# Kernel tuning notes

Measured on AMD Instinct MI355X. Metric: run time of the kernel, lower is better.

## Reference

```python
import jax, jax.numpy as jnp
import numpy as np

B, T, IN_DIM, OUT_DIM, H = 4096, 256, 64, 32, 128

def _linear_params(key, out_f, in_f):
    k1, k2 = jax.random.split(key)
    bound = 1.0 / np.sqrt(in_f)
    W = jax.random.uniform(k1, (out_f, in_f), jnp.float32, -bound, bound)
    b = jax.random.uniform(k2, (out_f,), jnp.float32, -bound, bound)
    return W, b

def _lstm_params(key, input_sz, hidden_sz):
    ks = jax.random.split(key, 4)
    bound = 1.0 / np.sqrt(hidden_sz)
    Wih = jax.random.uniform(ks[0], (4 * hidden_sz, input_sz), jnp.float32, -bound, bound)
    Whh = jax.random.uniform(ks[1], (4 * hidden_sz, hidden_sz), jnp.float32, -bound, bound)
    bih = jax.random.uniform(ks[2], (4 * hidden_sz,), jnp.float32, -bound, bound)
    bhh = jax.random.uniform(ks[3], (4 * hidden_sz,), jnp.float32, -bound, bound)
    return Wih, Whh, bih, bhh

def setup_inputs() -> dict:
    key = jax.random.key(0)
    ks = jax.random.split(key, 9)
    seq = jax.random.normal(ks[0], (B, T, IN_DIM), jnp.float32)
    h1 = jnp.zeros((B, H), jnp.float32); c1 = jnp.zeros((B, H), jnp.float32)
    h2 = jnp.zeros((B, H), jnp.float32); c2 = jnp.zeros((B, H), jnp.float32)
    W_in1, b_in1 = _linear_params(ks[1], 256, IN_DIM)
    W_in2, b_in2 = _linear_params(ks[2], 128, 256)
    W_in3, b_in3 = _linear_params(ks[3], 128, 128)
    Wih1, Whh1, bih1, bhh1 = _lstm_params(ks[4], 128, H)
    Wih2, Whh2, bih2, bhh2 = _lstm_params(ks[5], 128, H)
    W_out1, b_out1 = _linear_params(ks[6], 128, 128)
    W_out2, b_out2 = _linear_params(ks[7], 256, 128)
    W_out3, b_out3 = _linear_params(ks[8], OUT_DIM, 256)
    return dict(seq=seq, h1=h1, c1=c1, h2=h2, c2=c2,
                W_in1=W_in1, b_in1=b_in1, W_in2=W_in2, b_in2=b_in2, W_in3=W_in3, b_in3=b_in3,
                Wih1=Wih1, Whh1=Whh1, bih1=bih1, bhh1=bhh1,
                Wih2=Wih2, Whh2=Whh2, bih2=bih2, bhh2=bhh2,
                W_out1=W_out1, b_out1=b_out1, W_out2=W_out2, b_out2=b_out2, W_out3=W_out3, b_out3=b_out3)

def _lstm_cell(x, h, c, Wih, Whh, bih, bhh):
    # PyTorch LSTMCell: gates ordered i, f, g, o
    g = x @ Wih.T + bih + h @ Whh.T + bhh
    i, f, gg, o = jnp.split(g, 4, axis=-1)
    c_new = jax.nn.sigmoid(f) * c + jax.nn.sigmoid(i) * jnp.tanh(gg)
    h_new = jax.nn.sigmoid(o) * jnp.tanh(c_new)
    return h_new, c_new

def reference(seq, h1, c1, h2, c2,
              W_in1, b_in1, W_in2, b_in2, W_in3, b_in3,
              Wih1, Whh1, bih1, bhh1, Wih2, Whh2, bih2, bhh2,
              W_out1, b_out1, W_out2, b_out2, W_out3, b_out3):
    # fc_in applied to all timesteps at once (same math as per-step)
    x = jax.nn.relu(seq @ W_in1.T + b_in1)
    x = jax.nn.relu(x @ W_in2.T + b_in2)
    x = jax.nn.relu(x @ W_in3.T + b_in3)  # [B, T, 128]

    def step(carry, xt):
        h1, c1, h2, c2 = carry
        h1, c1 = _lstm_cell(xt, h1, c1, Wih1, Whh1, bih1, bhh1)
        h2, c2 = _lstm_cell(h1, h2, c2, Wih2, Whh2, bih2, bhh2)
        return (h1, c1, h2, c2), None

    (h1, c1, h2, c2), _ = jax.lax.scan(step, (h1, c1, h2, c2), jnp.swapaxes(x, 0, 1))

    y = jax.nn.relu(h2 @ W_out1.T + b_out1)
    y = jax.nn.relu(y @ W_out2.T + b_out2)
    return y @ W_out3.T + b_out3  # [B, out_dim]
```

## Files before the change

### kernel.cpp

```cpp
#include <hip/hip_runtime.h>


typedef unsigned short u16;
typedef short bf16x8 __attribute__((ext_vector_type(8)));
typedef float f32x4 __attribute__((ext_vector_type(4)));
typedef unsigned short u16x4 __attribute__((ext_vector_type(4)));

#define MFMA16(a, b, c) __builtin_amdgcn_mfma_f32_16x16x32_bf16((a), (b), (c), 0, 0, 0)

#define GLOAD_LDS(gp, lp) __builtin_amdgcn_global_load_lds( \
    (const __attribute__((address_space(1))) unsigned int*)(const void*)(gp), \
    (__attribute__((address_space(3))) unsigned int*)(void*)(lp), 16, 0, 0)

#define LGKM_BAR do { \
  asm volatile("s_waitcnt lgkmcnt(0)" ::: "memory"); \
  __builtin_amdgcn_sched_barrier(0); \
  __builtin_amdgcn_s_barrier(); \
  __builtin_amdgcn_sched_barrier(0); \
} while (0)

__device__ __forceinline__ u16 f2bf(float f) {
  union { float f; unsigned u; } v; v.f = f;
  return (u16)((v.u + 0x7FFFu + ((v.u >> 16) & 1u)) >> 16);
}
__device__ __forceinline__ float b2f(u16 v) {
  union { unsigned u; float f; } x; x.u = ((unsigned)v) << 16; return x.f;
}
__device__ __forceinline__ float fsig(float x) {
  return __builtin_amdgcn_rcpf(1.0f + __expf(-x));
}
__device__ __forceinline__ float ftanh(float x) {
  return 2.0f * __builtin_amdgcn_rcpf(1.0f + __expf(-2.0f * x)) - 1.0f;
}

#define WHH1_U  0
#define WIH2_U  65536
#define WHH2_U  131072
#define WIH1_U  196608
#define W1_U    262144
#define W2_U    278528
#define W3_U    311296
#define WO1_U   327680
#define WO2_U   344064
#define WO3_U   376832
#define BS1_F   192512
#define BS2_F   193024
#define STH1_U  393216
#define STH2_U  917504
#define C1_F    720896
#define C2_F    1245184
#define G1X_U   4194304
#define TC      32
#define NCH     8


__global__ void prep_kernel(const float* __restrict__ Wih1, const float* __restrict__ Whh1,
                            const float* __restrict__ bih1, const float* __restrict__ bhh1,
                            const float* __restrict__ Wih2, const float* __restrict__ Whh2,
                            const float* __restrict__ bih2, const float* __restrict__ bhh2,
                            const float* __restrict__ W_in1, const float* __restrict__ W_in2,
                            const float* __restrict__ W_in3,
                            const float* __restrict__ W_out1, const float* __restrict__ W_out2,
                            const float* __restrict__ W_out3,
                            const float* __restrict__ h1_in, const float* __restrict__ h2_in,
                            const float* __restrict__ c1_in, const float* __restrict__ c2_in,
                            u16* __restrict__ wsu) {
  float* wsf = (float*)wsu;
  const int N_total = 2490368;
  int stride = gridDim.x * blockDim.x;
  for (int idx = blockIdx.x * blockDim.x + threadIdx.x; idx < N_total; idx += stride) {
    if (idx < 385024) {
      int within = idx & 511;
      int f = idx >> 9;
      int lane = within >> 3, e = within & 7;
      int lr = lane & 15, lg = lane >> 4;
      int k8 = lg * 8 + e;
      float v;
      if (f < 128) {
        int kf = f & 3, g = (f >> 2) & 3, w = f >> 4;
        v = Whh1[(g * 128 + w * 16 + lr) * 128 + kf * 32 + k8];
      } else if (f < 256) {
        int ff = f - 128; int kf = ff & 3, g = (ff >> 2) & 3, w = ff >> 4;
        v = Wih2[(g * 128 + w * 16 + lr) * 128 + kf * 32 + k8];
      } else if (f < 384) {
        int ff = f - 256; int kf = ff & 3, g = (ff >> 2) & 3, w = ff >> 4;
        v = Whh2[(g * 128 + w * 16 + lr) * 128 + kf * 32 + k8];
      } else if (f < 512) {
        int ff = f - 384; int kf = ff & 3, n = ff >> 2;
        v = Wih1[(n * 16 + lr) * 128 + kf * 32 + k8];
      } else if (f < 544) {
        int ff = f - 512; int kf = ff & 1, n = ff >> 1;
        v = W_in1[(n * 16 + lr) * 64 + kf * 32 + k8];
      } else if (f < 608) {
        int ff = f - 544; int kf = ff & 7, n = ff >> 3;
        v = W_in2[(n * 16 + lr) * 256 + kf * 32 + k8];
      } else if (f < 640) {
        int ff = f - 608; int kf = ff & 3, n = ff >> 2;
        v = W_in3[(n * 16 + lr) * 128 + kf * 32 + k8];
      } else if (f < 672) {
        int ff = f - 640; int kf = ff & 3, n = ff >> 2;
        v = W_out1[(n * 16 + lr) * 128 + kf * 32 + k8];
      } else if (f < 736) {
        int ff = f - 672; int kf = ff & 3, n = ff >> 2;
        v = W_out2[(n * 16 + lr) * 128 + kf * 32 + k8];
      } else {
        int ff = f - 736; int kf = ff & 7, n = ff >> 3;
        v = W_out3[(n * 16 + lr) * 256 + kf * 32 + k8];
      }
      wsu[idx] = f2bf(v);
    } else if (idx < 385536) {
      int i = idx - 385024; wsf[BS1_F + i] = bih1[i] + bhh1[i];
    } else if (idx < 386048) {
      int i = idx - 385536; wsf[BS2_F + i] = bih2[i] + bhh2[i];
    } else if (idx < 393216) {
    } else if (idx < 917504) {
      int i = idx - 393216; wsu[STH1_U + i] = f2bf(h1_in[i]);
    } else if (idx < 1441792) {
      int i = idx - 917504; wsu[STH2_U + i] = f2bf(h2_in[i]);
    } else if (idx < 1966080) {
      int i = idx - 1441792; wsf[C1_F + i] = c1_in[i];
    } else {
      int i = idx - 1966080; wsf[C2_F + i] = c2_in[i];
    }
  }
}

__global__ __launch_bounds__(256, 2)
void fc_chunk(const float* __restrict__ seq,
              const float* __restrict__ b_in1, const float* __restrict__ b_in2,
              const float* __restrict__ b_in3,
              u16* __restrict__ wsu, int t0) {
  __shared__ u16 SEQs[4096];
  __shared__ u16 F1s[16384];
  __shared__ u16 F2s[8192];
  __shared__ u16 XLs[8192];
  const int tid = threadIdx.x;
  const int wid = tid >> 6, lane = tid & 63;
  const int lr = lane & 15, lg = lane >> 4;
  const int bid_t = blockIdx.x & 1, bid_b = blockIdx.x >> 1;
  const int b0c = bid_b * 4, t0c = t0 + bid_t * 16;
  const float* bs1f = (const float*)wsu + BS1_F;

#pragma unroll
  for (int i = 0; i < 4; ++i) {
    int f = i * 1024 + tid * 4;
    int rho = f >> 6, k = f & 63;
    int b = b0c + (rho >> 4), tt = t0c + (rho & 15);
    float4 v = *(const float4*)(seq + ((size_t)b * 256 + tt) * 64 + k);
    u16x4 o = { f2bf(v.x), f2bf(v.y), f2bf(v.z), f2bf(v.w) };
    *(u16x4*)&SEQs[(rho * 64 + k) ^ ((rho & 7) << 3)] = o;
  }
  __syncthreads();

  {
    f32x4 a1[4][4] = {};
#pragma unroll
    for (int kf = 0; kf < 2; ++kf) {
      bf16x8 A[4];
#pragma unroll
      for (int rt = 0; rt < 4; ++rt) {
        int r = 16 * rt + lr;
        A[rt] = *(const bf16x8*)&SEQs[(r * 64 + (kf * 4 + lg) * 8) ^ ((r & 7) << 3)];
      }
#pragma unroll
      for (int n = 0; n < 4; ++n) {
        bf16x8 B = *(const bf16x8*)(wsu + W1_U + (size_t)(((4 * wid + n) * 2 + kf) * 512) + lane * 8);
#pragma unroll
        for (int rt = 0; rt < 4; ++rt) a1[rt][n] = MFMA16(A[rt], B, a1[rt][n]);
      }
    }
#pragma unroll
    for (int n = 0; n < 4; ++n) {
      float bb = b_in1[(4 * wid + n) * 16 + lr];
#pragma unroll
      for (int rt = 0; rt < 4; ++rt)
#pragma unroll
        for (int j = 0; j < 4; ++j) {
          int r = 16 * rt + lg * 4 + j, c = (4 * wid + n) * 16 + lr;
          F1s[(r * 256 + c) ^ ((r & 7) << 3)] = f2bf(fmaxf(a1[rt][n][j] + bb, 0.f));
        }
    }
  }
  __syncthreads();

  {
    f32x4 a2[4][2] = {};
#pragma unroll
    for (int kf = 0; kf < 8; ++kf) {
      bf16x8 A[4];
#pragma unroll
      for (int rt = 0; rt < 4; ++rt) {
        int r = 16 * rt + lr;
        A[rt] = *(const bf16x8*)&F1s[(r * 256 + (kf * 4 + lg) * 8) ^ ((r & 7) << 3)];
      }
#pragma unroll
      for (int n = 0; n < 2; ++n) {
        bf16x8 B = *(const bf16x8*)(wsu + W2_U + (size_t)(((2 * wid + n) * 8 + kf) * 512) + lane * 8);
#pragma unroll
        for (int rt = 0; rt < 4; ++rt) a2[rt][n] = MFMA16(A[rt], B, a2[rt][n]);
      }
    }
#pragma unroll
    for (int n = 0; n < 2; ++n) {
      float bb = b_in2[(2 * wid + n) * 16 + lr];
#pragma unroll
      for (int rt = 0; rt < 4; ++rt)
#pragma unroll
        for (int j = 0; j < 4; ++j) {
          int r = 16 * rt + lg * 4 + j, c = (2 * wid + n) * 16 + lr;
          F2s[(r * 128 + c) ^ ((r & 7) << 3)] = f2bf(fmaxf(a2[rt][n][j] + bb, 0.f));
        }
    }
  }
  __syncthreads();

  {
    f32x4 a3[4][2] = {};
#pragma unroll
    for (int kf = 0; kf < 4; ++kf) {
      bf16x8 A[4];
#pragma unroll
      for (int rt = 0; rt < 4; ++rt) {
        int r = 16 * rt + lr;
        A[rt] = *(const bf16x8*)&F2s[(r * 128 + (kf * 4 + lg) * 8) ^ ((r & 7) << 3)];
      }
#pragma unroll
      for (int n = 0; n < 2; ++n) {
        bf16x8 B = *(const bf16x8*)(wsu + W3_U + (size_t)(((2 * wid + n) * 4 + kf) * 512) + lane * 8);
#pragma unroll
        for (int rt = 0; rt < 4; ++rt) a3[rt][n] = MFMA16(A[rt], B, a3[rt][n]);
      }
    }
#pragma unroll
    for (int n = 0; n < 2; ++n) {
      float bb = b_in3[(2 * wid + n) * 16 + lr];
#pragma unroll
      for (int rt = 0; rt < 4; ++rt)
#pragma unroll
        for (int j = 0; j < 4; ++j) {
          int r = 16 * rt + lg * 4 + j, c = (2 * wid + n) * 16 + lr;
          XLs[(r * 128 + c) ^ ((r & 7) << 3)] = f2bf(fmaxf(a3[rt][n][j] + bb, 0.f));
        }
    }
  }
  __syncthreads();

  {
    f32x4 a4[4][8] = {};
#pragma unroll
    for (int kf = 0; kf < 4; ++kf) {
      bf16x8 A[4];
#pragma unroll
      for (int rt = 0; rt < 4; ++rt) {
        int r = 16 * rt + lr;
        A[rt] = *(const bf16x8*)&XLs[(r * 128 + (kf * 4 + lg) * 8) ^ ((r & 7) << 3)];
      }
#pragma unroll
      for (int n = 0; n < 8; ++n) {
        bf16x8 B = *(const bf16x8*)(wsu + WIH1_U + (size_t)(((wid * 8 + n) * 4 + kf) * 512) + lane * 8);
#pragma unroll
        for (int rt = 0; rt < 4; ++rt) a4[rt][n] = MFMA16(A[rt], B, a4[rt][n]);
      }
    }
    const int blk = bid_b >> 2, slg = bid_b & 3;
#pragma unroll
    for (int n = 0; n < 8; ++n) {
      float bb = bs1f[(wid * 8 + n) * 16 + lr];
#pragma unroll
      for (int j = 0; j < 4; ++j) {
        int tl = bid_t * 16 + lg * 4 + j;
        u16x4 o = { f2bf(a4[0][n][j] + bb), f2bf(a4[1][n][j] + bb),
                    f2bf(a4[2][n][j] + bb), f2bf(a4[3][n][j] + bb) };
        size_t au = (size_t)G1X_U +
            ((((((size_t)tl * 256 + blk) * 4 + slg) * 4 + wid) * 8 + n) * 16 + lr) * 4;
        *(u16x4*)(wsu + au) = o;
      }
    }
  }
}

__global__ __launch_bounds__(512, 1)
void scan_chunk(u16* __restrict__ wsu, float* __restrict__ out,
                const float* __restrict__ b_out1, const float* __restrict__ b_out2,
                const float* __restrict__ b_out3, int last) {
  __shared__ u16 Wl[65536];
  __shared__ u16 H1d[2][2048], H2d[2][2048];

  float* wsf = (float*)wsu;
  const int tid = threadIdx.x;
  const int wid = tid >> 6, lane = tid & 63;
  const int lr = lane & 15, lg = lane >> 4;
  const int b0 = blockIdx.x * 16;
  const int blkid = blockIdx.x;
  const int r5 = tid >> 5, c5 = (tid & 31) * 4;
  const int swl = (r5 * 128 + c5) ^ ((r5 & 7) << 3);

  bf16x8 wA[4][4], wB[4][4];
#pragma unroll
  for (int g = 0; g < 4; ++g)
#pragma unroll
    for (int kf = 0; kf < 4; ++kf) {
      wA[g][kf] = *(const bf16x8*)(wsu + WHH1_U + (size_t)(((wid * 4 + g) * 4 + kf) * 512) + lane * 8);
      wB[g][kf] = *(const bf16x8*)(wsu + WIH2_U + (size_t)(((wid * 4 + g) * 4 + kf) * 512) + lane * 8);
    }
#pragma unroll
  for (int g = 0; g < 4; ++g)
#pragma unroll
    for (int kf = 0; kf < 4; ++kf) {
      asm volatile("" : "+a"(wA[g][kf]));
      asm volatile("" : "+a"(wB[g][kf]));
    }

#pragma unroll
  for (int i = 0; i < 16; ++i)
    GLOAD_LDS(wsu + WHH2_U + (wid * 16 + i) * 512 + lane * 8, &Wl[(wid * 16 + i) * 512]);

  *(u16x4*)&H1d[0][swl] = *(const u16x4*)(wsu + STH1_U + (size_t)(b0 + r5) * 128 + c5);
  *(u16x4*)&H2d[0][swl] = *(const u16x4*)(wsu + STH2_U + (size_t)(b0 + r5) * 128 + c5);
  float cs1[4], cs2[4], bc2[4];
#pragma unroll
  for (int j = 0; j < 4; ++j) {
    cs1[j] = wsf[C1_F + (size_t)(b0 + lg * 4 + j) * 128 + 16 * wid + lr];
    cs2[j] = wsf[C2_F + (size_t)(b0 + lg * 4 + j) * 128 + 16 * wid + lr];
  }
#pragma unroll
  for (int g = 0; g < 4; ++g) bc2[g] = wsf[BS2_F + g * 128 + 16 * wid + lr];

  u16x4 gx[4];
#pragma unroll
  for (int g = 0; g < 4; ++g)
    gx[g] = *(const u16x4*)(wsu + G1X_U +
        ((((((size_t)0 * 256 + blkid) * 4 + lg) * 4 + g) * 8 + wid) * 16 + lr) * 4);

  __syncthreads();

  auto frag = [&](const u16* buf, int kg) -> bf16x8 {
    return *(const bf16x8*)&buf[(lr * 128 + kg * 8) ^ ((lr & 7) << 3)];
  };

#pragma unroll 2
  for (int tl = 0; tl < TC; ++tl) {
    const int p = tl & 1, q = p ^ 1;

    f32x4 acc[4];
#pragma unroll
    for (int g = 0; g < 4; ++g)
      acc[g] = (f32x4){ b2f(gx[g][0]), b2f(gx[g][1]), b2f(gx[g][2]), b2f(gx[g][3]) };
    if (tl < TC - 1) {
#pragma unroll
      for (int g = 0; g < 4; ++g)
        gx[g] = *(const u16x4*)(wsu + G1X_U +
            ((((((size_t)(tl + 1) * 256 + blkid) * 4 + lg) * 4 + g) * 8 + wid) * 16 + lr) * 4);
    }
    bf16x8 h1f[4];
#pragma unroll
    for (int kf = 0; kf < 4; ++kf) h1f[kf] = frag(H1d[p], kf * 4 + lg);
#pragma unroll
    for (int kf = 0; kf < 4; ++kf)
#pragma unroll
      for (int g = 0; g < 4; ++g) acc[g] = MFMA16(h1f[kf], wA[g][kf], acc[g]);
    u16 hv[4];
#pragma unroll
    for (int j = 0; j < 4; ++j) {
      float cn = fsig(acc[1][j]) * cs1[j] + fsig(acc[0][j]) * ftanh(acc[2][j]);
      cs1[j] = cn;
      hv[j] = f2bf(fsig(acc[3][j]) * ftanh(cn));
    }
#pragma unroll
    for (int j = 0; j < 4; ++j) {
      int r = lg * 4 + j;
      H1d[q][(r * 128 + 16 * wid + lr) ^ ((r & 7) << 3)] = hv[j];
    }
    LGKM_BAR;

    f32x4 acd[4];
#pragma unroll
    for (int g = 0; g < 4; ++g) acd[g] = (f32x4){ bc2[g], bc2[g], bc2[g], bc2[g] };
#pragma unroll
    for (int kf = 0; kf < 4; ++kf) {
      bf16x8 h1n = frag(H1d[q], kf * 4 + lg);
#pragma unroll
      for (int g = 0; g < 4; ++g) acd[g] = MFMA16(h1n, wB[g][kf], acd[g]);
    }
#pragma unroll
    for (int kf = 0; kf < 4; ++kf) {
      bf16x8 h2f = frag(H2d[p], kf * 4 + lg);
#pragma unroll
      for (int g = 0; g < 4; ++g) {
        bf16x8 B = *(const bf16x8*)&Wl[(((wid * 4 + g) * 4 + kf) * 512) + lane * 8];
        acd[g] = MFMA16(h2f, B, acd[g]);
      }
    }
#pragma unroll
    for (int j = 0; j < 4; ++j) {
      float cn = fsig(acd[1][j]) * cs2[j] + fsig(acd[0][j]) * ftanh(acd[2][j]);
      cs2[j] = cn;
      hv[j] = f2bf(fsig(acd[3][j]) * ftanh(cn));
    }
#pragma unroll
    for (int j = 0; j < 4; ++j) {
      int r = lg * 4 + j;
      H2d[q][(r * 128 + 16 * wid + lr) ^ ((r & 7) << 3)] = hv[j];
    }
  }
  LGKM_BAR;

  if (!last) {
    *(u16x4*)(wsu + STH1_U + (size_t)(b0 + r5) * 128 + c5) = *(const u16x4*)&H1d[0][swl];
    *(u16x4*)(wsu + STH2_U + (size_t)(b0 + r5) * 128 + c5) = *(const u16x4*)&H2d[0][swl];
#pragma unroll
    for (int j = 0; j < 4; ++j) {
      wsf[C1_F + (size_t)(b0 + lg * 4 + j) * 128 + 16 * wid + lr] = cs1[j];
      wsf[C2_F + (size_t)(b0 + lg * 4 + j) * 128 + 16 * wid + lr] = cs2[j];
    }
  } else {
    {
      f32x4 y1 = {};
#pragma unroll
      for (int kf = 0; kf < 4; ++kf) {
        bf16x8 A = frag(H2d[0], kf * 4 + lg);
        bf16x8 B = *(const bf16x8*)(wsu + WO1_U + (size_t)((wid * 4 + kf) * 512) + lane * 8);
        y1 = MFMA16(A, B, y1);
      }
      float bo1 = b_out1[wid * 16 + lr];
      LGKM_BAR;
#pragma unroll
      for (int j = 0; j < 4; ++j) {
        int r = lg * 4 + j;
        H1d[1][(r * 128 + 16 * wid + lr) ^ ((r & 7) << 3)] = f2bf(fmaxf(y1[j] + bo1, 0.f));
      }
      LGKM_BAR;
    }
    {
      f32x4 y2[2] = {};
#pragma unroll
      for (int kf = 0; kf < 4; ++kf) {
        bf16x8 A = frag(H1d[1], kf * 4 + lg);
#pragma unroll
        for (int n = 0; n < 2; ++n) {
          bf16x8 B = *(const bf16x8*)(wsu + WO2_U + (size_t)(((2 * wid + n) * 4 + kf) * 512) + lane * 8);
          y2[n] = MFMA16(A, B, y2[n]);
        }
      }
      LGKM_BAR;
#pragma unroll
      for (int n = 0; n < 2; ++n)
#pragma unroll
        for (int j = 0; j < 4; ++j) {
          int c = (2 * wid + n) * 16 + lr;
          float v = fmaxf(y2[n][j] + b_out2[c], 0.f);
          u16* buf = (c < 128) ? &H2d[1][0] : &H1d[0][0];
          int cc = c & 127, r = lg * 4 + j;
          buf[(r * 128 + cc) ^ ((r & 7) << 3)] = f2bf(v);
        }
      LGKM_BAR;
    }
    if (wid < 2) {
      f32x4 y3 = {};
#pragma unroll
      for (int kf = 0; kf < 8; ++kf) {
        const u16* ab = (kf < 4) ? &H2d[1][0] : &H1d[0][0];
        bf16x8 A = frag(ab, (kf & 3) * 4 + lg);
        bf16x8 B = *(const bf16x8*)(wsu + WO3_U + (size_t)((wid * 8 + kf) * 512) + lane * 8);
        y3 = MFMA16(A, B, y3);
      }
      float bo3 = b_out3[wid * 16 + lr];
#pragma unroll
      for (int j = 0; j < 4; ++j)
        out[(size_t)(b0 + lg * 4 + j) * 32 + wid * 16 + lr] = y3[j] + bo3;
    }
  }
}

extern "C" void kernel_launch(void* const* d_in, const int* in_sizes, int n_in,
                              void* d_out, int out_size, void* d_ws, size_t ws_size,
                              hipStream_t stream) {
  (void)in_sizes; (void)n_in; (void)out_size; (void)ws_size;
  const float* seq    = (const float*)d_in[0];
  const float* h1     = (const float*)d_in[1];
  const float* c1     = (const float*)d_in[2];
  const float* h2     = (const float*)d_in[3];
  const float* c2     = (const float*)d_in[4];
  const float* W_in1  = (const float*)d_in[5];
  const float* b_in1  = (const float*)d_in[6];
  const float* W_in2  = (const float*)d_in[7];
  const float* b_in2  = (const float*)d_in[8];
  const float* W_in3  = (const float*)d_in[9];
  const float* b_in3  = (const float*)d_in[10];
  const float* Wih1   = (const float*)d_in[11];
  const float* Whh1   = (const float*)d_in[12];
  const float* bih1   = (const float*)d_in[13];
  const float* bhh1   = (const float*)d_in[14];
  const float* Wih2   = (const float*)d_in[15];
  const float* Whh2   = (const float*)d_in[16];
  const float* bih2   = (const float*)d_in[17];
  const float* bhh2   = (const float*)d_in[18];
  const float* W_out1 = (const float*)d_in[19];
  const float* b_out1 = (const float*)d_in[20];
  const float* W_out2 = (const float*)d_in[21];
  const float* b_out2 = (const float*)d_in[22];
  const float* W_out3 = (const float*)d_in[23];
  const float* b_out3 = (const float*)d_in[24];
  u16* wsu = (u16*)d_ws;
  float* out = (float*)d_out;

  hipLaunchKernelGGL(prep_kernel, dim3(512), dim3(256), 0, stream,
                     Wih1, Whh1, bih1, bhh1, Wih2, Whh2, bih2, bhh2,
                     W_in1, W_in2, W_in3, W_out1, W_out2, W_out3,
                     h1, h2, c1, c2, wsu);
  for (int k = 0; k < NCH; ++k) {
    hipLaunchKernelGGL(fc_chunk, dim3(2048), dim3(256), 0, stream,
                       seq, b_in1, b_in2, b_in3, wsu, k * TC);
    hipLaunchKernelGGL(scan_chunk, dim3(256), dim3(512), 0, stream,
                       wsu, out, b_out1, b_out2, b_out3, (k == NCH - 1) ? 1 : 0);
  }
}
```

Measured before the change: 1.669 ms.

## Fuse FC and scan chunks into one kernel overlapping next-chunk FC with scan

```diff
diff --git a/kernel.cpp b/kernel.cpp
--- a/kernel.cpp
+++ b/kernel.cpp
@@ -50,9 +50,8 @@
 #define C1_F    720896
 #define C2_F    1245184
 #define G1X_U   4194304
+#define G1X_SLOT 67108864
 #define TC      32
-#define NCH     8
-
 
 __global__ void prep_kernel(const float* __restrict__ Wih1, const float* __restrict__ Whh1,
                             const float* __restrict__ bih1, const float* __restrict__ bhh1,
@@ -125,349 +124,401 @@
   }
 }
 
-__global__ __launch_bounds__(256, 2)
-void fc_chunk(const float* __restrict__ seq,
-              const float* __restrict__ b_in1, const float* __restrict__ b_in2,
-              const float* __restrict__ b_in3,
-              u16* __restrict__ wsu, int t0) {
-  __shared__ u16 SEQs[4096];
-  __shared__ u16 F1s[16384];
-  __shared__ u16 F2s[8192];
-  __shared__ u16 XLs[8192];
-  const int tid = threadIdx.x;
-  const int wid = tid >> 6, lane = tid & 63;
-  const int lr = lane & 15, lg = lane >> 4;
-  const int bid_t = blockIdx.x & 1, bid_b = blockIdx.x >> 1;
-  const int b0c = bid_b * 4, t0c = t0 + bid_t * 16;
-  const float* bs1f = (const float*)wsu + BS1_F;
-
-#pragma unroll
-  for (int i = 0; i < 4; ++i) {
-    int f = i * 1024 + tid * 4;
-    int rho = f >> 6, k = f & 63;
-    int b = b0c + (rho >> 4), tt = t0c + (rho & 15);
-    float4 v = *(const float4*)(seq + ((size_t)b * 256 + tt) * 64 + k);
-    u16x4 o = { f2bf(v.x), f2bf(v.y), f2bf(v.z), f2bf(v.w) };
-    *(u16x4*)&SEQs[(rho * 64 + k) ^ ((rho & 7) << 3)] = o;
-  }
-  __syncthreads();
-
-  {
-    f32x4 a1[4][4] = {};
-#pragma unroll
-    for (int kf = 0; kf < 2; ++kf) {
-      bf16x8 A[4];
-#pragma unroll
-      for (int rt = 0; rt < 4; ++rt) {
-        int r = 16 * rt + lr;
-        A[rt] = *(const bf16x8*)&SEQs[(r * 64 + (kf * 4 + lg) * 8) ^ ((r & 7) << 3)];
-      }
-#pragma unroll
-      for (int n = 0; n < 4; ++n) {
-        bf16x8 B = *(const bf16x8*)(wsu + W1_U + (size_t)(((4 * wid + n) * 2 + kf) * 512) + lane * 8);
-#pragma unroll
-        for (int rt = 0; rt < 4; ++rt) a1[rt][n] = MFMA16(A[rt], B, a1[rt][n]);
-      }
-    }
-#pragma unroll
-    for (int n = 0; n < 4; ++n) {
-      float bb = b_in1[(4 * wid + n) * 16 + lr];
-#pragma unroll
-      for (int rt = 0; rt < 4; ++rt)
-#pragma unroll
-        for (int j = 0; j < 4; ++j) {
-          int r = 16 * rt + lg * 4 + j, c = (4 * wid + n) * 16 + lr;
-          F1s[(r * 256 + c) ^ ((r & 7) << 3)] = f2bf(fmaxf(a1[rt][n][j] + bb, 0.f));
-        }
-    }
-  }
-  __syncthreads();
-
-  {
-    f32x4 a2[4][2] = {};
-#pragma unroll
-    for (int kf = 0; kf < 8; ++kf) {
-      bf16x8 A[4];
-#pragma unroll
-      for (int rt = 0; rt < 4; ++rt) {
-        int r = 16 * rt + lr;
-        A[rt] = *(const bf16x8*)&F1s[(r * 256 + (kf * 4 + lg) * 8) ^ ((r & 7) << 3)];
-      }
-#pragma unroll
-      for (int n = 0; n < 2; ++n) {
-        bf16x8 B = *(const bf16x8*)(wsu + W2_U + (size_t)(((2 * wid + n) * 8 + kf) * 512) + lane * 8);
-#pragma unroll
-        for (int rt = 0; rt < 4; ++rt) a2[rt][n] = MFMA16(A[rt], B, a2[rt][n]);
-      }
-    }
-#pragma unroll
-    for (int n = 0; n < 2; ++n) {
-      float bb = b_in2[(2 * wid + n) * 16 + lr];
-#pragma unroll
-      for (int rt = 0; rt < 4; ++rt)
-#pragma unroll
-        for (int j = 0; j < 4; ++j) {
-          int r = 16 * rt + lg * 4 + j, c = (2 * wid + n) * 16 + lr;
-          F2s[(r * 128 + c) ^ ((r & 7) << 3)] = f2bf(fmaxf(a2[rt][n][j] + bb, 0.f));
-        }
-    }
-  }
-  __syncthreads();
-
-  {
-    f32x4 a3[4][2] = {};
-#pragma unroll
-    for (int kf = 0; kf < 4; ++kf) {
-      bf16x8 A[4];
-#pragma unroll
-      for (int rt = 0; rt < 4; ++rt) {
-        int r = 16 * rt + lr;
-        A[rt] = *(const bf16x8*)&F2s[(r * 128 + (kf * 4 + lg) * 8) ^ ((r & 7) << 3)];
-      }
-#pragma unroll
-      for (int n = 0; n < 2; ++n) {
-        bf16x8 B = *(const bf16x8*)(wsu + W3_U + (size_t)(((2 * wid + n) * 4 + kf) * 512) + lane * 8);
-#pragma unroll
-        for (int rt = 0; rt < 4; ++rt) a3[rt][n] = MFMA16(A[rt], B, a3[rt][n]);
-      }
-    }
-#pragma unroll
-    for (int n = 0; n < 2; ++n) {
-      float bb = b_in3[(2 * wid + n) * 16 + lr];
-#pragma unroll
-      for (int rt = 0; rt < 4; ++rt)
-#pragma unroll
-        for (int j = 0; j < 4; ++j) {
-          int r = 16 * rt + lg * 4 + j, c = (2 * wid + n) * 16 + lr;
-          XLs[(r * 128 + c) ^ ((r & 7) << 3)] = f2bf(fmaxf(a3[rt][n][j] + bb, 0.f));
-        }
-    }
-  }
-  __syncthreads();
-
-  {
-    f32x4 a4[4][8] = {};
-#pragma unroll
-    for (int kf = 0; kf < 4; ++kf) {
-      bf16x8 A[4];
-#pragma unroll
-      for (int rt = 0; rt < 4; ++rt) {
-        int r = 16 * rt + lr;
-        A[rt] = *(const bf16x8*)&XLs[(r * 128 + (kf * 4 + lg) * 8) ^ ((r & 7) << 3)];
-      }
-#pragma unroll
-      for (int n = 0; n < 8; ++n) {
-        bf16x8 B = *(const bf16x8*)(wsu + WIH1_U + (size_t)(((wid * 8 + n) * 4 + kf) * 512) + lane * 8);
-#pragma unroll
-        for (int rt = 0; rt < 4; ++rt) a4[rt][n] = MFMA16(A[rt], B, a4[rt][n]);
-      }
-    }
-    const int blk = bid_b >> 2, slg = bid_b & 3;
-#pragma unroll
-    for (int n = 0; n < 8; ++n) {
-      float bb = bs1f[(wid * 8 + n) * 16 + lr];
-#pragma unroll
-      for (int j = 0; j < 4; ++j) {
-        int tl = bid_t * 16 + lg * 4 + j;
-        u16x4 o = { f2bf(a4[0][n][j] + bb), f2bf(a4[1][n][j] + bb),
-                    f2bf(a4[2][n][j] + bb), f2bf(a4[3][n][j] + bb) };
-        size_t au = (size_t)G1X_U +
-            ((((((size_t)tl * 256 + blk) * 4 + slg) * 4 + wid) * 8 + n) * 16 + lr) * 4;
-        *(u16x4*)(wsu + au) = o;
-      }
-    }
-  }
-}
-
 __global__ __launch_bounds__(512, 1)
-void scan_chunk(u16* __restrict__ wsu, float* __restrict__ out,
-                const float* __restrict__ b_out1, const float* __restrict__ b_out2,
-                const float* __restrict__ b_out3, int last) {
-  __shared__ u16 Wl[65536];
-  __shared__ u16 H1d[2][2048], H2d[2][2048];
-
+void fused_kernel(const float* __restrict__ seq,
+                  const float* __restrict__ b_in1, const float* __restrict__ b_in2,
+                  const float* __restrict__ b_in3,
+                  const float* __restrict__ b_out1, const float* __restrict__ b_out2,
+                  const float* __restrict__ b_out3,
+                  u16* __restrict__ wsu, float* __restrict__ out,
+                  int nscan, int scan_chunk, int fc_chunk, int last) {
+  __shared__ u16 SH[77824];
   float* wsf = (float*)wsu;
   const int tid = threadIdx.x;
-  const int wid = tid >> 6, lane = tid & 63;
-  const int lr = lane & 15, lg = lane >> 4;
-  const int b0 = blockIdx.x * 16;
-  const int blkid = blockIdx.x;
-  const int r5 = tid >> 5, c5 = (tid & 31) * 4;
-  const int swl = (r5 * 128 + c5) ^ ((r5 & 7) << 3);
-
-  bf16x8 wA[4][4], wB[4][4];
-#pragma unroll
-  for (int g = 0; g < 4; ++g)
-#pragma unroll
-    for (int kf = 0; kf < 4; ++kf) {
-      wA[g][kf] = *(const bf16x8*)(wsu + WHH1_U + (size_t)(((wid * 4 + g) * 4 + kf) * 512) + lane * 8);
-      wB[g][kf] = *(const bf16x8*)(wsu + WIH2_U + (size_t)(((wid * 4 + g) * 4 + kf) * 512) + lane * 8);
-    }
-#pragma unroll
-  for (int g = 0; g < 4; ++g)
-#pragma unroll
-    for (int kf = 0; kf < 4; ++kf) {
-      asm volatile("" : "+a"(wA[g][kf]));
-      asm volatile("" : "+a"(wB[g][kf]));
-    }
-
-#pragma unroll
-  for (int i = 0; i < 16; ++i)
-    GLOAD_LDS(wsu + WHH2_U + (wid * 16 + i) * 512 + lane * 8, &Wl[(wid * 16 + i) * 512]);
-
-  *(u16x4*)&H1d[0][swl] = *(const u16x4*)(wsu + STH1_U + (size_t)(b0 + r5) * 128 + c5);
-  *(u16x4*)&H2d[0][swl] = *(const u16x4*)(wsu + STH2_U + (size_t)(b0 + r5) * 128 + c5);
-  float cs1[4], cs2[4], bc2[4];
-#pragma unroll
-  for (int j = 0; j < 4; ++j) {
-    cs1[j] = wsf[C1_F + (size_t)(b0 + lg * 4 + j) * 128 + 16 * wid + lr];
-    cs2[j] = wsf[C2_F + (size_t)(b0 + lg * 4 + j) * 128 + 16 * wid + lr];
-  }
-#pragma unroll
-  for (int g = 0; g < 4; ++g) bc2[g] = wsf[BS2_F + g * 128 + 16 * wid + lr];
-
-  u16x4 gx[4];
-#pragma unroll
-  for (int g = 0; g < 4; ++g)
-    gx[g] = *(const u16x4*)(wsu + G1X_U +
-        ((((((size_t)0 * 256 + blkid) * 4 + lg) * 4 + g) * 8 + wid) * 16 + lr) * 4);
-
-  __syncthreads();
-
-  auto frag = [&](const u16* buf, int kg) -> bf16x8 {
-    return *(const bf16x8*)&buf[(lr * 128 + kg * 8) ^ ((lr & 7) << 3)];
-  };
+  const int bid = blockIdx.x;
+
+  if (bid < nscan) {
+    u16* WL  = SH;
+    u16* H1D = SH + 65536;
+    u16* H2S = SH + 73728;
+    const int wid = tid >> 6, lane = tid & 63;
+    const int lr = lane & 15, lg = lane >> 4;
+    const int b0 = bid * 32;
+
+    bf16x8 wA[4][4], wB[4][4];
+#pragma unroll
+    for (int g = 0; g < 4; ++g)
+#pragma unroll
+      for (int kf = 0; kf < 4; ++kf) {
+        size_t fo = (size_t)(((wid * 4 + g) * 4 + kf) * 512) + lane * 8;
+        wA[g][kf] = *(const bf16x8*)(wsu + WHH1_U + fo);
+        wB[g][kf] = *(const bf16x8*)(wsu + WIH2_U + fo);
+      }
+#pragma unroll
+    for (int g = 0; g < 4; ++g)
+#pragma unroll
+      for (int kf = 0; kf < 4; ++kf) {
+        asm volatile("" : "+a"(wA[g][kf]));
+        asm volatile("" : "+a"(wB[g][kf]));
+      }
+#pragma unroll
+    for (int i = 0; i < 16; ++i)
+      GLOAD_LDS(wsu + WHH2_U + (wid * 16 + i) * 512 + lane * 8, &WL[(wid * 16 + i) * 512]);
+
+    const int srow = tid >> 4, sg8 = tid & 15;
+    const int sws = (srow * 128 + sg8 * 8) ^ ((srow & 7) << 3);
+    *(bf16x8*)&H1D[sws] = *(const bf16x8*)(wsu + STH1_U + (size_t)(b0 + srow) * 128 + sg8 * 8);
+    *(bf16x8*)&H2S[sws] = *(const bf16x8*)(wsu + STH2_U + (size_t)(b0 + srow) * 128 + sg8 * 8);
+    float cs1[2][4], cs2[2][4], bc2[4];
+#pragma unroll
+    for (int rt = 0; rt < 2; ++rt)
+#pragma unroll
+      for (int j = 0; j < 4; ++j) {
+        size_t off = (size_t)(b0 + 16 * rt + lg * 4 + j) * 128 + 16 * wid + lr;
+        cs1[rt][j] = wsf[C1_F + off];
+        cs2[rt][j] = wsf[C2_F + off];
+      }
+#pragma unroll
+    for (int g = 0; g < 4; ++g) bc2[g] = wsf[BS2_F + g * 128 + 16 * wid + lr];
+
+    const u16* gp = wsu + G1X_U + (size_t)(scan_chunk & 1) * G1X_SLOT +
+                    (size_t)(2 * bid) * 8192 + lg * 2048 + wid * 64 + lr * 4;
+    u16x4 gx[2][4];
+#pragma unroll
+    for (int rt = 0; rt < 2; ++rt)
+#pragma unroll
+      for (int g = 0; g < 4; ++g)
+        gx[rt][g] = *(const u16x4*)(gp + rt * 8192 + g * 512);
+
+    __syncthreads();
+
+    auto frag = [&](const u16* buf, int rt, int kg) -> bf16x8 {
+      return *(const bf16x8*)&buf[((16 * rt + lr) * 128 + kg * 8) ^ ((lr & 7) << 3)];
+    };
 
 #pragma unroll 2
-  for (int tl = 0; tl < TC; ++tl) {
-    const int p = tl & 1, q = p ^ 1;
-
-    f32x4 acc[4];
-#pragma unroll
-    for (int g = 0; g < 4; ++g)
-      acc[g] = (f32x4){ b2f(gx[g][0]), b2f(gx[g][1]), b2f(gx[g][2]), b2f(gx[g][3]) };
-    if (tl < TC - 1) {
-#pragma unroll
-      for (int g = 0; g < 4; ++g)
-        gx[g] = *(const u16x4*)(wsu + G1X_U +
-            ((((((size_t)(tl + 1) * 256 + blkid) * 4 + lg) * 4 + g) * 8 + wid) * 16 + lr) * 4);
-    }
-    bf16x8 h1f[4];
-#pragma unroll
-    for (int kf = 0; kf < 4; ++kf) h1f[kf] = frag(H1d[p], kf * 4 + lg);
-#pragma unroll
-    for (int kf = 0; kf < 4; ++kf)
-#pragma unroll
-      for (int g = 0; g < 4; ++g) acc[g] = MFMA16(h1f[kf], wA[g][kf], acc[g]);
-    u16 hv[4];
-#pragma unroll
-    for (int j = 0; j < 4; ++j) {
-      float cn = fsig(acc[1][j]) * cs1[j] + fsig(acc[0][j]) * ftanh(acc[2][j]);
-      cs1[j] = cn;
-      hv[j] = f2bf(fsig(acc[3][j]) * ftanh(cn));
-    }
-#pragma unroll
-    for (int j = 0; j < 4; ++j) {
-      int r = lg * 4 + j;
-      H1d[q][(r * 128 + 16 * wid + lr) ^ ((r & 7) << 3)] = hv[j];
+    for (int tl = 0; tl < TC; ++tl) {
+      const int p = tl & 1, q = p ^ 1;
+      u16* H1p = H1D + p * 4096;
+      u16* H1q = H1D + q * 4096;
+
+      f32x4 acc[2][4];
+#pragma unroll
+      for (int rt = 0; rt < 2; ++rt)
+#pragma unroll
+        for (int g = 0; g < 4; ++g)
+          acc[rt][g] = (f32x4){ b2f(gx[rt][g][0]), b2f(gx[rt][g][1]),
+                                b2f(gx[rt][g][2]), b2f(gx[rt][g][3]) };
+      if (tl < TC - 1) {
+        const u16* gpt = gp + (size_t)(tl + 1) * 2097152;
+#pragma unroll
+        for (int rt = 0; rt < 2; ++rt)
+#pragma unroll
+          for (int g = 0; g < 4; ++g)
+            gx[rt][g] = *(const u16x4*)(gpt + rt * 8192 + g * 512);
+      }
+#pragma unroll
+      for (int kf = 0; kf < 4; ++kf) {
+        bf16x8 a0 = frag(H1p, 0, kf * 4 + lg);
+        bf16x8 a1 = frag(H1p, 1, kf * 4 + lg);
+#pragma unroll
+        for (int g = 0; g < 4; ++g) {
+          acc[0][g] = MFMA16(a0, wA[g][kf], acc[0][g]);
+          acc[1][g] = MFMA16(a1, wA[g][kf], acc[1][g]);
+        }
+      }
+#pragma unroll
+      for (int rt = 0; rt < 2; ++rt)
+#pragma unroll
+        for (int j = 0; j < 4; ++j) {
+          float cn = fsig(acc[rt][1][j]) * cs1[rt][j] + fsig(acc[rt][0][j]) * ftanh(acc[rt][2][j]);
+          cs1[rt][j] = cn;
+          int r = 16 * rt + lg * 4 + j;
+          H1q[(r * 128 + 16 * wid + lr) ^ ((r & 7) << 3)] = f2bf(fsig(acc[rt][3][j]) * ftanh(cn));
+        }
+      LGKM_BAR;
+
+      f32x4 acd[2][4];
+#pragma unroll
+      for (int rt = 0; rt < 2; ++rt)
+#pragma unroll
+        for (int g = 0; g < 4; ++g)
+          acd[rt][g] = (f32x4){ bc2[g], bc2[g], bc2[g], bc2[g] };
+#pragma unroll
+      for (int kf = 0; kf < 4; ++kf) {
+        bf16x8 a0 = frag(H1q, 0, kf * 4 + lg);
+        bf16x8 a1 = frag(H1q, 1, kf * 4 + lg);
+#pragma unroll
+        for (int g = 0; g < 4; ++g) {
+          acd[0][g] = MFMA16(a0, wB[g][kf], acd[0][g]);
+          acd[1][g] = MFMA16(a1, wB[g][kf], acd[1][g]);
+        }
+      }
+#pragma unroll
+      for (int kf = 0; kf < 4; ++kf) {
+        bf16x8 h0 = frag(H2S, 0, kf * 4 + lg);
+        bf16x8 h1 = frag(H2S, 1, kf * 4 + lg);
+#pragma unroll
+        for (int g = 0; g < 4; ++g) {
+          bf16x8 B = *(const bf16x8*)&WL[(((wid * 4 + g) * 4 + kf) * 512) + lane * 8];
+          acd[0][g] = MFMA16(h0, B, acd[0][g]);
+          acd[1][g] = MFMA16(h1, B, acd[1][g]);
+        }
+      }
+      u16 hv[2][4];
+#pragma unroll
+      for (int rt = 0; rt < 2; ++rt)
+#pragma unroll
+        for (int j = 0; j < 4; ++j) {
+          float cn = fsig(acd[rt][1][j]) * cs2[rt][j] + fsig(acd[rt][0][j]) * ftanh(acd[rt][2][j]);
+          cs2[rt][j] = cn;
+          hv[rt][j] = f2bf(fsig(acd[rt][3][j]) * ftanh(cn));
+        }
+      LGKM_BAR;
+#pragma unroll
+      for (int rt = 0; rt < 2; ++rt)
+#pragma unroll
+        for (int j = 0; j < 4; ++j) {
+          int r = 16 * rt + lg * 4 + j;
+          H2S[(r * 128 + 16 * wid + lr) ^ ((r & 7) << 3)] = hv[rt][j];
+        }
     }
     LGKM_BAR;
 
-    f32x4 acd[4];
-#pragma unroll
-    for (int g = 0; g < 4; ++g) acd[g] = (f32x4){ bc2[g], bc2[g], bc2[g], bc2[g] };
-#pragma unroll
-    for (int kf = 0; kf < 4; ++kf) {
-      bf16x8 h1n = frag(H1d[q], kf * 4 + lg);
-#pragma unroll
-      for (int g = 0; g < 4; ++g) acd[g] = MFMA16(h1n, wB[g][kf], acd[g]);
-    }
-#pragma unroll
-    for (int kf = 0; kf < 4; ++kf) {
-      bf16x8 h2f = frag(H2d[p], kf * 4 + lg);
-#pragma unroll
-      for (int g = 0; g < 4; ++g) {
-        bf16x8 B = *(const bf16x8*)&Wl[(((wid * 4 + g) * 4 + kf) * 512) + lane * 8];
-        acd[g] = MFMA16(h2f, B, acd[g]);
-      }
-    }
-#pragma unroll
-    for (int j = 0; j < 4; ++j) {
-      float cn = fsig(acd[1][j]) * cs2[j] + fsig(acd[0][j]) * ftanh(acd[2][j]);
-      cs2[j] = cn;
-      hv[j] = f2bf(fsig(acd[3][j]) * ftanh(cn));
-    }
-#pragma unroll
-    for (int j = 0; j < 4; ++j) {
-      int r = lg * 4 + j;
-      H2d[q][(r * 128 + 16 * wid + lr) ^ ((r & 7) << 3)] = hv[j];
-    }
-  }
-  LGKM_BAR;
-
-  if (!last) {
-    *(u16x4*)(wsu + STH1_U + (size_t)(b0 + r5) * 128 + c5) = *(const u16x4*)&H1d[0][swl];
-    *(u16x4*)(wsu + STH2_U + (size_t)(b0 + r5) * 128 + c5) = *(const u16x4*)&H2d[0][swl];
-#pragma unroll
-    for (int j = 0; j < 4; ++j) {
-      wsf[C1_F + (size_t)(b0 + lg * 4 + j) * 128 + 16 * wid + lr] = cs1[j];
-      wsf[C2_F + (size_t)(b0 + lg * 4 + j) * 128 + 16 * wid + lr] = cs2[j];
+    if (!last) {
+      *(bf16x8*)(wsu + STH1_U + (size_t)(b0 + srow) * 128 + sg8 * 8) = *(const bf16x8*)&H1D[sws];
+      *(bf16x8*)(wsu + STH2_U + (size_t)(b0 + srow) * 128 + sg8 * 8) = *(const bf16x8*)&H2S[sws];
+#pragma unroll
+      for (int rt = 0; rt < 2; ++rt)
+#pragma unroll
+        for (int j = 0; j < 4; ++j) {
+          size_t off = (size_t)(b0 + 16 * rt + lg * 4 + j) * 128 + 16 * wid + lr;
+          wsf[C1_F + off] = cs1[rt][j];
+          wsf[C2_F + off] = cs2[rt][j];
+        }
+    } else {
+      u16* Y1b  = H1D + 4096;
+      u16* Y2lo = H2S;
+      u16* Y2hi = H1D;
+      {
+        f32x4 y1[2] = {};
+#pragma unroll
+        for (int kf = 0; kf < 4; ++kf) {
+          bf16x8 B = *(const bf16x8*)(wsu + WO1_U + (size_t)((wid * 4 + kf) * 512) + lane * 8);
+          y1[0] = MFMA16(frag(H2S, 0, kf * 4 + lg), B, y1[0]);
+          y1[1] = MFMA16(frag(H2S, 1, kf * 4 + lg), B, y1[1]);
+        }
+        float bo1 = b_out1[wid * 16 + lr];
+        LGKM_BAR;
+#pragma unroll
+        for (int rt = 0; rt < 2; ++rt)
+#pragma unroll
+          for (int j = 0; j < 4; ++j) {
+            int r = 16 * rt + lg * 4 + j;
+            Y1b[(r * 128 + 16 * wid + lr) ^ ((r & 7) << 3)] = f2bf(fmaxf(y1[rt][j] + bo1, 0.f));
+          }
+        LGKM_BAR;
+      }
+      {
+        f32x4 y2[2][2] = {};
+#pragma unroll
+        for (int kf = 0; kf < 4; ++kf) {
+          bf16x8 a0 = frag(Y1b, 0, kf * 4 + lg);
+          bf16x8 a1 = frag(Y1b, 1, kf * 4 + lg);
+#pragma unroll
+          for (int n = 0; n < 2; ++n) {
+            bf16x8 B = *(const bf16x8*)(wsu + WO2_U + (size_t)(((2 * wid + n) * 4 + kf) * 512) + lane * 8);
+            y2[0][n] = MFMA16(a0, B, y2[0][n]);
+            y2[1][n] = MFMA16(a1, B, y2[1][n]);
+          }
+        }
+        LGKM_BAR;
+#pragma unroll
+        for (int rt = 0; rt < 2; ++rt)
+#pragma unroll
+          for (int n = 0; n < 2; ++n)
+#pragma unroll
+            for (int j = 0; j < 4; ++j) {
+              int c = (2 * wid + n) * 16 + lr;
+              float v = fmaxf(y2[rt][n][j] + b_out2[c], 0.f);
+              u16* buf = (c < 128) ? Y2lo : Y2hi;
+              int cc = c & 127, r = 16 * rt + lg * 4 + j;
+              buf[(r * 128 + cc) ^ ((r & 7) << 3)] = f2bf(v);
+            }
+        LGKM_BAR;
+      }
+      if (wid < 4) {
+        int rt = wid >> 1, ci = wid & 1;
+        f32x4 y3 = {};
+#pragma unroll
+        for (int kf = 0; kf < 8; ++kf) {
+          const u16* ab = (kf < 4) ? Y2lo : Y2hi;
+          bf16x8 A = frag(ab, rt, (kf & 3) * 4 + lg);
+          bf16x8 B = *(const bf16x8*)(wsu + WO3_U + (size_t)((ci * 8 + kf) * 512) + lane * 8);
+          y3 = MFMA16(A, B, y3);
+        }
+        float bo3 = b_out3[ci * 16 + lr];
+#pragma unroll
+        for (int j = 0; j < 4; ++j)
+          out[(size_t)(b0 + 16 * rt + lg * 4 + j) * 32 + ci * 16 + lr] = y3[j] + bo3;
+      }
     }
   } else {
-    {
-      f32x4 y1 = {};
-#pragma unroll
-      for (int kf = 0; kf < 4; ++kf) {
-        bf16x8 A = frag(H2d[0], kf * 4 + lg);
-        bf16x8 B = *(const bf16x8*)(wsu + WO1_U + (size_t)((wid * 4 + kf) * 512) + lane * 8);
-        y1 = MFMA16(A, B, y1);
-      }
-      float bo1 = b_out1[wid * 16 + lr];
-      LGKM_BAR;
-#pragma unroll
-      for (int j = 0; j < 4; ++j) {
-        int r = lg * 4 + j;
-        H1d[1][(r * 128 + 16 * wid + lr) ^ ((r & 7) << 3)] = f2bf(fmaxf(y1[j] + bo1, 0.f));
-      }
-      LGKM_BAR;
-    }
-    {
-      f32x4 y2[2] = {};
-#pragma unroll
-      for (int kf = 0; kf < 4; ++kf) {
-        bf16x8 A = frag(H1d[1], kf * 4 + lg);
+    const int sub = tid >> 8, stid = tid & 255;
+    u16* S = SH + sub * 36864;
+    u16* SEQs = S;
+    u16* F1s  = S + 4096;
+    u16* F2s  = S + 20480;
+    u16* XLs  = S + 28672;
+    const int wid = stid >> 6, lane = stid & 63;
+    const int lr = lane & 15, lg = lane >> 4;
+    const int t0 = fc_chunk * TC;
+    const size_t g1b = (size_t)G1X_U + (size_t)(fc_chunk & 1) * G1X_SLOT;
+    const float* bs1f = (const float*)wsu + BS1_F;
+    const int nunits = 2 * (gridDim.x - nscan);
+    const int unit = (bid - nscan) * 2 + sub;
+
+    for (int tile = unit; tile < 2048; tile += nunits) {
+      const int bid_t = tile & 1, bid_b = tile >> 1;
+      const int b0c = bid_b * 4, t0c = t0 + bid_t * 16;
+
+#pragma unroll
+      for (int i = 0; i < 4; ++i) {
+        int f = i * 1024 + stid * 4;
+        int rho = f >> 6, k = f & 63;
+        int b = b0c + (rho >> 4), tt = t0c + (rho & 15);
+        float4 v = *(const float4*)(seq + ((size_t)b * 256 + tt) * 64 + k);
+        u16x4 o = { f2bf(v.x), f2bf(v.y), f2bf(v.z), f2bf(v.w) };
+        *(u16x4*)&SEQs[(rho * 64 + k) ^ ((rho & 7) << 3)] = o;
+      }
+      __syncthreads();
+
+      {
+        f32x4 a1[4][4] = {};
+#pragma unroll
+        for (int kf = 0; kf < 2; ++kf) {
+          bf16x8 A[4];
+#pragma unroll
+          for (int rt = 0; rt < 4; ++rt) {
+            int r = 16 * rt + lr;
+            A[rt] = *(const bf16x8*)&SEQs[(r * 64 + (kf * 4 + lg) * 8) ^ ((r & 7) << 3)];
+          }
+#pragma unroll
+          for (int n = 0; n < 4; ++n) {
+            bf16x8 B = *(const bf16x8*)(wsu + W1_U + (size_t)(((4 * wid + n) * 2 + kf) * 512) + lane * 8);
+#pragma unroll
+            for (int rt = 0; rt < 4; ++rt) a1[rt][n] = MFMA16(A[rt], B, a1[rt][n]);
+          }
+        }
+#pragma unroll
+        for (int n = 0; n < 4; ++n) {
+          float bb = b_in1[(4 * wid + n) * 16 + lr];
+#pragma unroll
+          for (int rt = 0; rt < 4; ++rt)
+#pragma unroll
+            for (int j = 0; j < 4; ++j) {
+              int r = 16 * rt + lg * 4 + j, c = (4 * wid + n) * 16 + lr;
+              F1s[(r * 256 + c) ^ ((r & 7) << 3)] = f2bf(fmaxf(a1[rt][n][j] + bb, 0.f));
+            }
+        }
+      }
+      __syncthreads();
+
+      {
+        f32x4 a2[4][2] = {};
+#pragma unroll
+        for (int kf = 0; kf < 8; ++kf) {
+          bf16x8 A[4];
+#pragma unroll
+          for (int rt = 0; rt < 4; ++rt) {
+            int r = 16 * rt + lr;
+            A[rt] = *(const bf16x8*)&F1s[(r * 256 + (kf * 4 + lg) * 8) ^ ((r & 7) << 3)];
+          }
+#pragma unroll
+          for (int n = 0; n < 2; ++n) {
+            bf16x8 B = *(const bf16x8*)(wsu + W2_U + (size_t)(((2 * wid + n) * 8 + kf) * 512) + lane * 8);
+#pragma unroll
+            for (int rt = 0; rt < 4; ++rt) a2[rt][n] = MFMA16(A[rt], B, a2[rt][n]);
+          }
+        }
 #pragma unroll
         for (int n = 0; n < 2; ++n) {
-          bf16x8 B = *(const bf16x8*)(wsu + WO2_U + (size_t)(((2 * wid + n) * 4 + kf) * 512) + lane * 8);
-          y2[n] = MFMA16(A, B, y2[n]);
-        }
-      }
-      LGKM_BAR;
-#pragma unroll
-      for (int n = 0; n < 2; ++n)
-#pragma unroll
-        for (int j = 0; j < 4; ++j) {
-          int c = (2 * wid + n) * 16 + lr;
-          float v = fmaxf(y2[n][j] + b_out2[c], 0.f);
-          u16* buf = (c < 128) ? &H2d[1][0] : &H1d[0][0];
-          int cc = c & 127, r = lg * 4 + j;
-          buf[(r * 128 + cc) ^ ((r & 7) << 3)] = f2bf(v);
-        }
-      LGKM_BAR;
-    }
-    if (wid < 2) {
-      f32x4 y3 = {};
-#pragma unroll
-      for (int kf = 0; kf < 8; ++kf) {
-        const u16* ab = (kf < 4) ? &H2d[1][0] : &H1d[0][0];
-        bf16x8 A = frag(ab, (kf & 3) * 4 + lg);
-        bf16x8 B = *(const bf16x8*)(wsu + WO3_U + (size_t)((wid * 8 + kf) * 512) + lane * 8);
-        y3 = MFMA16(A, B, y3);
-      }
-      float bo3 = b_out3[wid * 16 + lr];
-#pragma unroll
-      for (int j = 0; j < 4; ++j)
-        out[(size_t)(b0 + lg * 4 + j) * 32 + wid * 16 + lr] = y3[j] + bo3;
+          float bb = b_in2[(2 * wid + n) * 16 + lr];
+#pragma unroll
+          for (int rt = 0; rt < 4; ++rt)
+#pragma unroll
+            for (int j = 0; j < 4; ++j) {
+              int r = 16 * rt + lg * 4 + j, c = (2 * wid + n) * 16 + lr;
+              F2s[(r * 128 + c) ^ ((r & 7) << 3)] = f2bf(fmaxf(a2[rt][n][j] + bb, 0.f));
+            }
+        }
+      }
+      __syncthreads();
+
+      {
+        f32x4 a3[4][2] = {};
+#pragma unroll
+        for (int kf = 0; kf < 4; ++kf) {
+          bf16x8 A[4];
+#pragma unroll
+          for (int rt = 0; rt < 4; ++rt) {
+            int r = 16 * rt + lr;
+            A[rt] = *(const bf16x8*)&F2s[(r * 128 + (kf * 4 + lg) * 8) ^ ((r & 7) << 3)];
+          }
+#pragma unroll
+          for (int n = 0; n < 2; ++n) {
+            bf16x8 B = *(const bf16x8*)(wsu + W3_U + (size_t)(((2 * wid + n) * 4 + kf) * 512) + lane * 8);
+#pragma unroll
+            for (int rt = 0; rt < 4; ++rt) a3[rt][n] = MFMA16(A[rt], B, a3[rt][n]);
+          }
+        }
+#pragma unroll
+        for (int n = 0; n < 2; ++n) {
+          float bb = b_in3[(2 * wid + n) * 16 + lr];
+#pragma unroll
+          for (int rt = 0; rt < 4; ++rt)
+#pragma unroll
+            for (int j = 0; j < 4; ++j) {
+              int r = 16 * rt + lg * 4 + j, c = (2 * wid + n) * 16 + lr;
+              XLs[(r * 128 + c) ^ ((r & 7) << 3)] = f2bf(fmaxf(a3[rt][n][j] + bb, 0.f));
+            }
+        }
+      }
+      __syncthreads();
+
+      {
+        f32x4 a4[4][8] = {};
+#pragma unroll
+        for (int kf = 0; kf < 4; ++kf) {
+          bf16x8 A[4];
+#pragma unroll
+          for (int rt = 0; rt < 4; ++rt) {
+            int r = 16 * rt + lr;
+            A[rt] = *(const bf16x8*)&XLs[(r * 128 + (kf * 4 + lg) * 8) ^ ((r & 7) << 3)];
+          }
+#pragma unroll
+          for (int n = 0; n < 8; ++n) {
+            bf16x8 B = *(const bf16x8*)(wsu + WIH1_U + (size_t)(((wid * 8 + n) * 4 + kf) * 512) + lane * 8);
+#pragma unroll
+            for (int rt = 0; rt < 4; ++rt) a4[rt][n] = MFMA16(A[rt], B, a4[rt][n]);
+          }
+        }
+        const int blk = bid_b >> 2, slg = bid_b & 3;
+#pragma unroll
+        for (int n = 0; n < 8; ++n) {
+          float bb = bs1f[(wid * 8 + n) * 16 + lr];
+#pragma unroll
+          for (int j = 0; j < 4; ++j) {
+            int tl = bid_t * 16 + lg * 4 + j;
+            u16x4 o = { f2bf(a4[0][n][j] + bb), f2bf(a4[1][n][j] + bb),
+                        f2bf(a4[2][n][j] + bb), f2bf(a4[3][n][j] + bb) };
+            size_t au = g1b +
+                ((((((size_t)tl * 256 + blk) * 4 + slg) * 4 + wid) * 8 + n) * 16 + lr) * 4;
+            *(u16x4*)(wsu + au) = o;
+          }
+        }
+      }
+      __syncthreads();
     }
   }
 }
@@ -508,10 +559,14 @@
                      Wih1, Whh1, bih1, bhh1, Wih2, Whh2, bih2, bhh2,
                      W_in1, W_in2, W_in3, W_out1, W_out2, W_out3,
                      h1, h2, c1, c2, wsu);
-  for (int k = 0; k < NCH; ++k) {
-    hipLaunchKernelGGL(fc_chunk, dim3(2048), dim3(256), 0, stream,
-                       seq, b_in1, b_in2, b_in3, wsu, k * TC);
-    hipLaunchKernelGGL(scan_chunk, dim3(256), dim3(512), 0, stream,
-                       wsu, out, b_out1, b_out2, b_out3, (k == NCH - 1) ? 1 : 0);
-  }
-}
+  hipLaunchKernelGGL(fused_kernel, dim3(128), dim3(512), 0, stream,
+                     seq, b_in1, b_in2, b_in3, b_out1, b_out2, b_out3,
+                     wsu, out, 0, 0, 0, 0);
+  for (int k = 0; k < 7; ++k)
+    hipLaunchKernelGGL(fused_kernel, dim3(256), dim3(512), 0, stream,
+                       seq, b_in1, b_in2, b_in3, b_out1, b_out2, b_out3,
+                       wsu, out, 128, k, k + 1, 0);
+  hipLaunchKernelGGL(fused_kernel, dim3(128), dim3(512), 0, stream,
+                     seq, b_in1, b_in2, b_in3, b_out1, b_out2, b_out3,
+                     wsu, out, 128, 7, 0, 1);
+}
```

New measurement: 4.040 ms. 2.42x slower.
